# Optimization experiments

Measured on AMD Instinct MI355X. Metric: run time of the kernel, lower is better.

Reference implementation:

```python
import jax, jax.numpy as jnp
import numpy as np

B, T, N, C = 32, 12, 1024, 2   # batch, lookback window, n_series, in_channels
D, H, K, OUT = 16, 64, 2, 12   # embedding_dim, rnn_units, cheb_k, out_dim (horizon)


def setup_inputs() -> dict:
    key = jax.random.key(0)
    ks = jax.random.split(key, 12)
    p = lambda k, sh, s=0.1: jax.random.normal(k, sh, dtype=jnp.float32) * s
    return {
        "source": jax.random.normal(ks[0], (B, T, N, C), dtype=jnp.float32),
        "node_emb": p(ks[1], (N, D), 0.3),
        # layer 0: dim_in = C + H
        "gate_w0": p(ks[2], (D, K, C + H, 2 * H)),
        "gate_b0": p(ks[3], (D, 2 * H)),
        "upd_w0": p(ks[4], (D, K, C + H, H)),
        "upd_b0": p(ks[5], (D, H)),
        # layer 1: dim_in = H + H
        "gate_w1": p(ks[6], (D, K, 2 * H, 2 * H)),
        "gate_b1": p(ks[7], (D, 2 * H)),
        "upd_w1": p(ks[8], (D, K, 2 * H, H)),
        "upd_b1": p(ks[9], (D, H)),
        # end_conv: Conv2d(1, OUT*out_channels, kernel=(1,H)) == linear over hidden dim
        "conv_w": p(ks[10], (OUT, H)),
        "conv_b": p(ks[11], (OUT,)),
    }


def _supports(node_emb):
    # softmax(relu(E E^T)) row-normalized adaptive adjacency; Chebyshev stack (K, N, N)
    A = jax.nn.softmax(jax.nn.relu(node_emb @ node_emb.T), axis=1)
    s = [jnp.eye(N, dtype=A.dtype), A]
    for _ in range(2, K):
        s.append(2.0 * A @ s[-1] - s[-2])
    return jnp.stack(s, axis=0)


def _gcn(x, node_emb, w_pool, b_pool, supports):
    # x: (B, N, Cin); per-node adaptive weights from pools
    w = jnp.einsum('nd,dkio->nkio', node_emb, w_pool)     # (N, K, Cin, Cout)
    b = node_emb @ b_pool                                 # (N, Cout)
    xg = jnp.einsum('knm,bmc->bnkc', supports, x)         # (B, N, K, Cin)
    return jnp.einsum('bnki,nkio->bno', xg, w) + b


def _layer(x_seq, node_emb, supports, gw, gb, uw, ub):
    # x_seq: (B, T, N, Cin) -> (B, T, N, H) via GRU-style AGCRN cell, scanned over T
    def step(state, x_t):
        inp = jnp.concatenate([x_t, state], axis=-1)
        zr = jax.nn.sigmoid(_gcn(inp, node_emb, gw, gb, supports))
        z, r = jnp.split(zr, 2, axis=-1)
        cand = jnp.concatenate([x_t, z * state], axis=-1)
        hc = jnp.tanh(_gcn(cand, node_emb, uw, ub, supports))
        h = r * state + (1.0 - r) * hc
        return h, h

    init = jnp.zeros((x_seq.shape[0], N, H), dtype=x_seq.dtype)
    _, hs = jax.lax.scan(step, init, jnp.swapaxes(x_seq, 0, 1))
    return jnp.swapaxes(hs, 0, 1)


def reference(source, node_emb, gate_w0, gate_b0, upd_w0, upd_b0,
              gate_w1, gate_b1, upd_w1, upd_b1, conv_w, conv_b,
              teacher_forcing_ratio=0):
    sup = _supports(node_emb)  # adaptive supports depend only on static node_emb
    h1 = _layer(source, node_emb, sup, gate_w0, gate_b0, upd_w0, upd_b0)
    h2 = _layer(h1, node_emb, sup, gate_w1, gate_b1, upd_w1, upd_b1)
    last = h2[:, -1]  # (B, N, H)
    # end_conv over hidden dim -> (B, OUT, N); out_channels==1 so squeeze folds away
    out = jnp.einsum('bnh,oh->bon', last, conv_w) + conv_b[None, :, None]
    return out
```

## Files before the change

kernel.cpp:

```cpp
#include <hip/hip_runtime.h>
#include <hip/hip_fp16.h>


typedef _Float16 f16x8 __attribute__((ext_vector_type(8)));
typedef _Float16 f16x4 __attribute__((ext_vector_type(4)));
typedef float f32x4 __attribute__((ext_vector_type(4)));

__global__ __launch_bounds__(256) void compute_A_kernel(const float* __restrict__ E,
                                                        __half* __restrict__ Ah) {
  int n = blockIdx.x;
  int tid = threadIdx.x;
  __shared__ float red[256];
  float en[16];
#pragma unroll
  for (int d = 0; d < 16; ++d) en[d] = E[n * 16 + d];
  float v[4];
#pragma unroll
  for (int q = 0; q < 4; ++q) {
    int m = tid + q * 256;
    const float* Em = E + m * 16;
    float dot = 0.f;
#pragma unroll
    for (int d = 0; d < 16; ++d) dot += en[d] * Em[d];
    v[q] = fmaxf(dot, 0.f);
  }
  float mx = fmaxf(fmaxf(v[0], v[1]), fmaxf(v[2], v[3]));
  red[tid] = mx; __syncthreads();
  for (int s = 128; s > 0; s >>= 1) { if (tid < s) red[tid] = fmaxf(red[tid], red[tid + s]); __syncthreads(); }
  mx = red[0];
  __syncthreads();
  float e[4], sum = 0.f;
#pragma unroll
  for (int q = 0; q < 4; ++q) { e[q] = expf(v[q] - mx); sum += e[q]; }
  red[tid] = sum; __syncthreads();
  for (int s = 128; s > 0; s >>= 1) { if (tid < s) red[tid] += red[tid + s]; __syncthreads(); }
  float inv = 1.f / red[0];
#pragma unroll
  for (int q = 0; q < 4; ++q) Ah[(size_t)n * 1024 + tid + q * 256] = __float2half(e[q] * inv);
}

__global__ void build_e16_kernel(const float* __restrict__ E, __half* __restrict__ E16) {
  int t = blockIdx.x * 256 + threadIdx.x;
  if (t >= 1024 * 32) return;
  int d = t & 31;
  E16[t] = (d < 16) ? __float2half(E[(t >> 5) * 16 + d]) : __half(0);
}

__global__ void pool_t16_kernel(const float* __restrict__ gw0, const float* __restrict__ uw0,
                                const float* __restrict__ gw1, const float* __restrict__ uw1,
                                __half* __restrict__ poolT16) {
  int t = blockIdx.x * 256 + threadIdx.x;
  if (t >= 79872 * 32) return;
  int d = t & 31, j = t >> 5;
  if (d >= 16) { poolT16[t] = __half(0); return; }
  const float* pool; int F, Fp, O, loc;
  if (j < 20480)      { pool = gw0; F = 66;  Fp = 80;  O = 128; loc = j; }
  else if (j < 30720) { pool = uw0; F = 66;  Fp = 80;  O = 64;  loc = j - 20480; }
  else if (j < 63488) { pool = gw1; F = 128; Fp = 128; O = 128; loc = j - 30720; }
  else                { pool = uw1; F = 128; Fp = 128; O = 64;  loc = j - 63488; }
  int KIp = 2 * Fp;
  int o = loc / KIp, kip = loc - o * KIp;
  int kk = (kip >= Fp) ? 1 : 0;
  int jj = kip - kk * Fp;
  int i;
  if (F == Fp) i = jj;
  else i = (jj < 64) ? jj + 2 : (jj < 66 ? jj - 64 : -1);
  poolT16[t] = (i >= 0) ? __float2half(pool[(((size_t)d * 2 + kk) * F + i) * O + o]) : __half(0);
}

__global__ __launch_bounds__(256) void make_wt_mfma_kernel(
    const __half* __restrict__ E16g, const __half* __restrict__ poolT16g,
    __half* __restrict__ WtG0, __half* __restrict__ WtU0,
    __half* __restrict__ WtG1, __half* __restrict__ WtU1) {
  __shared__ __align__(16) _Float16 Es[64][40];
  __shared__ __align__(16) _Float16 wbuf[64][264];
  const _Float16* E16 = (const _Float16*)E16g;
  const _Float16* pT = (const _Float16*)poolT16g;
  int bx = blockIdx.x;
  __half* Wt; int OK, jbase;
  if (bx < 80)       { Wt = WtG0; OK = 128 * 160; jbase = bx * 256; }
  else if (bx < 120) { Wt = WtU0; OK = 64 * 160;  jbase = (bx - 80) * 256; }
  else if (bx < 248) { Wt = WtG1; OK = 128 * 256; jbase = (bx - 120) * 256; }
  else               { Wt = WtU1; OK = 64 * 256;  jbase = (bx - 248) * 256; }
  int jglob0 = bx * 256;
  int n0 = blockIdx.y * 64;
  {
    int r = threadIdx.x >> 2, ch = (threadIdx.x & 3) * 8;
    *(f16x8*)&Es[r][ch] = *(const f16x8*)(E16 + (size_t)(n0 + r) * 32 + ch);
  }
  __syncthreads();
  int wave = threadIdx.x >> 6, lane = threadIdx.x & 63;
  int fm = lane & 15, fg = lane >> 4;
  f16x8 af[4];
#pragma unroll
  for (int i = 0; i < 4; ++i) af[i] = *(const f16x8*)&Es[i * 16 + fm][fg * 8];
  f32x4 acc[4][4] = {};
#pragma unroll
  for (int j = 0; j < 4; ++j) {
    int jc = jglob0 + wave * 64 + j * 16 + fm;
    f16x8 bf = *(const f16x8*)(pT + (size_t)jc * 32 + fg * 8);
#pragma unroll
    for (int i = 0; i < 4; ++i)
      acc[i][j] = __builtin_amdgcn_mfma_f32_16x16x32_f16(af[i], bf, acc[i][j], 0, 0, 0);
  }
#pragma unroll
  for (int i = 0; i < 4; ++i)
#pragma unroll
    for (int j = 0; j < 4; ++j)
#pragma unroll
      for (int r = 0; r < 4; ++r)
        wbuf[i * 16 + fg * 4 + r][wave * 64 + j * 16 + fm] = (_Float16)acc[i][j][r];
  __syncthreads();
  for (int idx = threadIdx.x; idx < 64 * 32; idx += 256) {
    int nsub = idx >> 5, pos = (idx & 31) * 8;
    *(float4*)(Wt + (size_t)(n0 + nsub) * OK + jbase + pos) = *(float4*)&wbuf[nsub][pos];
  }
}

__global__ void make_b_all_kernel(const float* __restrict__ E,
                                  const float* __restrict__ gb0, const float* __restrict__ ub0,
                                  const float* __restrict__ gb1, const float* __restrict__ ub1,
                                  float* __restrict__ Bg0, float* __restrict__ Bu0,
                                  float* __restrict__ Bg1, float* __restrict__ Bu1) {
  int tid = blockIdx.x * 256 + threadIdx.x;
  if (tid >= 1024 * 384) return;
  int n = tid / 384, c = tid - n * 384;
  const float* pool; float* outp; int O, o;
  if (c < 128)      { pool = gb0; outp = Bg0; O = 128; o = c; }
  else if (c < 192) { pool = ub0; outp = Bu0; O = 64;  o = c - 128; }
  else if (c < 320) { pool = gb1; outp = Bg1; O = 128; o = c - 192; }
  else              { pool = ub1; outp = Bu1; O = 64;  o = c - 320; }
  const float* En = E + n * 16;
  float a = 0.f;
#pragma unroll
  for (int d = 0; d < 16; ++d) a += En[d] * pool[d * O + o];
  outp[n * O + o] = a;
}

__global__ void zero_kernel(float* __restrict__ p, int count) {
  int i = blockIdx.x * 256 + threadIdx.x;
  if (i < count) p[i] = 0.f;
}

__global__ void build_x16_kernel(const float* __restrict__ src, __half* __restrict__ x16) {
  int bid = blockIdx.x; int t = bid >> 5, b = bid & 31;
  const float* s = src + (size_t)(b * 12 + t) * 2048;
  __half* dst = x16 + t * 64 + b * 2;
  for (int n = threadIdx.x; n < 1024; n += 256) {
    float2 v = *(const float2*)(s + n * 2);
    *(__half2*)(dst + (size_t)n * 768) = __floats2half2_rn(v.x, v.y);
  }
}

__global__ __launch_bounds__(256) void gemm_nt_kernel(
    const __half* __restrict__ Ahg, const __half* __restrict__ X0g,
    const __half* __restrict__ X1g, __half* __restrict__ Yg,
    int Nc, int cstride, int split) {
  __shared__ __align__(16) _Float16 As[64][136];
  __shared__ __align__(16) _Float16 Bs[64][144];
  const _Float16* __restrict__ Ah = (const _Float16*)Ahg;
  _Float16* __restrict__ Y = (_Float16*)Yg;
  int tid = threadIdx.x;
  int row0 = blockIdx.y * 64;
  int col0 = blockIdx.x * 64;
  const _Float16* __restrict__ Xsrc =
      (col0 < split) ? (const _Float16*)X0g : (const _Float16*)X1g;
  int colg = (col0 < split) ? col0 : col0 - split;
  int wave = tid >> 6, lane = tid & 63;
  int wm = wave & 1, wn = wave >> 1;
  int fm = lane & 15, fg = lane >> 4;

  int sr = tid >> 2, sc = (tid & 3) * 32;
  const _Float16* pa = Ah + (size_t)(row0 + sr) * 1024 + sc;
  int kq = tid & 31, cg = tid >> 5;
  int kb = 4 * kq;
  const _Float16* pb = Xsrc + (size_t)kb * cstride + colg + cg * 8;
  int chunk = kq >> 1;
  int kin = (kq & 1) * 4;

  f16x8 ra[4], rb[4];
#pragma unroll
  for (int c = 0; c < 4; ++c) ra[c] = *(const f16x8*)(pa + c * 8);
#pragma unroll
  for (int r = 0; r < 4; ++r) rb[r] = *(const f16x8*)(pb + (size_t)r * cstride);

  f32x4 acc[2][2] = {};
  for (int k0 = 0; k0 < 1024; k0 += 128) {
#pragma unroll
    for (int c = 0; c < 4; ++c) *(f16x8*)&As[sr][sc + c * 8] = ra[c];
#pragma unroll
    for (int i = 0; i < 8; ++i) {
      int c = cg * 8 + i;
      f16x4 p;
      p[0] = rb[0][i]; p[1] = rb[1][i]; p[2] = rb[2][i]; p[3] = rb[3][i];
      *(f16x4*)&Bs[c][((chunk ^ (c & 7)) << 3) + kin] = p;
    }
    __syncthreads();
    if (k0 + 128 < 1024) {
#pragma unroll
      for (int c = 0; c < 4; ++c) ra[c] = *(const f16x8*)(pa + k0 + 128 + c * 8);
#pragma unroll
      for (int r = 0; r < 4; ++r)
        rb[r] = *(const f16x8*)(pb + (size_t)(k0 + 128 + r) * cstride);
    }
#pragma unroll
    for (int kc = 0; kc < 4; ++kc) {
      int ck = kc * 4 + fg;
      f16x8 af[2], bf[2];
#pragma unroll
      for (int i = 0; i < 2; ++i)
        af[i] = *(const f16x8*)&As[wm * 32 + i * 16 + fm][kc * 32 + fg * 8];
#pragma unroll
      for (int j = 0; j < 2; ++j) {
        int cl = wn * 32 + j * 16 + fm;
        bf[j] = *(const f16x8*)&Bs[cl][(ck ^ (cl & 7)) << 3];
      }
#pragma unroll
      for (int i = 0; i < 2; ++i)
#pragma unroll
        for (int j = 0; j < 2; ++j)
          acc[i][j] = __builtin_amdgcn_mfma_f32_16x16x32_f16(af[i], bf[j], acc[i][j], 0, 0, 0);
    }
    __syncthreads();
  }
#pragma unroll
  for (int i = 0; i < 2; ++i) {
#pragma unroll
    for (int j = 0; j < 2; ++j) {
      int col = col0 + wn * 32 + j * 16 + fm;
      int rbase = row0 + wm * 32 + i * 16 + fg * 4;
#pragma unroll
      for (int r = 0; r < 4; ++r)
        Y[(size_t)(rbase + r) * Nc + col] = (_Float16)acc[i][j][r];
    }
  }
}

__global__ __launch_bounds__(256) void gemm_nt128_kernel(
    const __half* __restrict__ Ahg, const __half* __restrict__ X0g,
    const __half* __restrict__ X1g, __half* __restrict__ Yg,
    int Nc, int cstride, int split) {
  __shared__ __align__(16) _Float16 As[64][136];
  __shared__ __align__(16) _Float16 Bs[128][144];
  const _Float16* __restrict__ Ah = (const _Float16*)Ahg;
  _Float16* __restrict__ Y = (_Float16*)Yg;
  int tid = threadIdx.x;
  int row0 = blockIdx.y * 64;
  int col0 = blockIdx.x * 128;
  const _Float16* __restrict__ Xsrc =
      (col0 < split) ? (const _Float16*)X0g : (const _Float16*)X1g;
  int colg = (col0 < split) ? col0 : col0 - split;
  int wave = tid >> 6, lane = tid & 63;
  int fm = lane & 15, fg = lane >> 4;

  int sr = tid >> 2, sc = (tid & 3) * 32;
  const _Float16* pa = Ah + (size_t)(row0 + sr) * 1024 + sc;
  int kq = tid & 31, cg = tid >> 5;
  int kb = 4 * kq;
  const _Float16* pb = Xsrc + (size_t)kb * cstride + colg + cg * 16;
  int chunk = kq >> 1;
  int kin = (kq & 1) * 4;

  f16x8 ra[4], rb[4][2];
#pragma unroll
  for (int c = 0; c < 4; ++c) ra[c] = *(const f16x8*)(pa + c * 8);
#pragma unroll
  for (int r = 0; r < 4; ++r)
#pragma unroll
    for (int h = 0; h < 2; ++h)
      rb[r][h] = *(const f16x8*)(pb + (size_t)r * cstride + h * 8);

  f32x4 acc[4][2] = {};
  for (int k0 = 0; k0 < 1024; k0 += 128) {
#pragma unroll
    for (int c = 0; c < 4; ++c) *(f16x8*)&As[sr][sc + c * 8] = ra[c];
#pragma unroll
    for (int h = 0; h < 2; ++h)
#pragma unroll
      for (int i = 0; i < 8; ++i) {
        int c = cg * 16 + h * 8 + i;
        f16x4 p;
        p[0] = rb[0][h][i]; p[1] = rb[1][h][i]; p[2] = rb[2][h][i]; p[3] = rb[3][h][i];
        *(f16x4*)&Bs[c][((chunk ^ (c & 7)) << 3) + kin] = p;
      }
    __syncthreads();
    if (k0 + 128 < 1024) {
#pragma unroll
      for (int c = 0; c < 4; ++c) ra[c] = *(const f16x8*)(pa + k0 + 128 + c * 8);
#pragma unroll
      for (int r = 0; r < 4; ++r)
#pragma unroll
        for (int h = 0; h < 2; ++h)
          rb[r][h] = *(const f16x8*)(pb + (size_t)(k0 + 128 + r) * cstride + h * 8);
    }
#pragma unroll
    for (int kc = 0; kc < 4; ++kc) {
      int ck = kc * 4 + fg;
      f16x8 af[4], bf[2];
#pragma unroll
      for (int i = 0; i < 4; ++i)
        af[i] = *(const f16x8*)&As[i * 16 + fm][kc * 32 + fg * 8];
#pragma unroll
      for (int j = 0; j < 2; ++j) {
        int cl = wave * 32 + j * 16 + fm;
        bf[j] = *(const f16x8*)&Bs[cl][(ck ^ (cl & 7)) << 3];
      }
#pragma unroll
      for (int i = 0; i < 4; ++i)
#pragma unroll
        for (int j = 0; j < 2; ++j)
          acc[i][j] = __builtin_amdgcn_mfma_f32_16x16x32_f16(af[i], bf[j], acc[i][j], 0, 0, 0);
    }
    __syncthreads();
  }
#pragma unroll
  for (int i = 0; i < 4; ++i) {
#pragma unroll
    for (int j = 0; j < 2; ++j) {
      int col = col0 + wave * 32 + j * 16 + fm;
      int rbase = row0 + i * 16 + fg * 4;
#pragma unroll
      for (int r = 0; r < 4; ++r)
        Y[(size_t)(rbase + r) * Nc + col] = (_Float16)acc[i][j][r];
    }
  }
}

__device__ __forceinline__ void gate0_body(
    _Float16* Xs, int n, int t,
    const __half* __restrict__ h16, const __half* __restrict__ YBD,
    const float* __restrict__ src, const __half* __restrict__ Axt, int tstep,
    const __half* __restrict__ Wtg, const float* __restrict__ Bg,
    const float* __restrict__ h32, __half* __restrict__ zh0, float* __restrict__ r0) {
  constexpr int KIP = 160, STRIDE = 168;
#pragma unroll
  for (int u = 0; u < 2; ++u) {
    int idx = t + u * 256;
    int b = idx >> 4, part = (idx >> 3) & 1, ch = idx & 7;
    const _Float16* s = part ? (const _Float16*)YBD + (size_t)n * 4096 + b * 64 + ch * 8
                             : (const _Float16*)h16 + (size_t)n * 2048 + b * 64 + ch * 8;
    *(f16x8*)&Xs[b * STRIDE + part * 80 + ch * 8] = *(const f16x8*)s;
  }
  if (t < 32) {
    int b = t;
    float2 xv = *(const float2*)(src + ((size_t)(b * 12 + tstep) * 1024 + n) * 2);
    Xs[b * STRIDE + 64] = (_Float16)xv.x;
    Xs[b * STRIDE + 65] = (_Float16)xv.y;
    const _Float16* ax = (const _Float16*)Axt + (size_t)n * 768 + tstep * 64 + b * 2;
    Xs[b * STRIDE + 144] = ax[0];
    Xs[b * STRIDE + 145] = ax[1];
  }
  for (int idx = t; idx < 896; idx += 256) {
    int b = idx / 28, jj = idx % 28;
    int col = (jj < 14) ? 66 + jj : 132 + jj;
    Xs[b * STRIDE + col] = (_Float16)0.f;
  }
  __syncthreads();
  int wave = t >> 6, lane = t & 63;
  int fm = lane & 15, fg = lane >> 4;
  f32x4 acc[2][2] = {};
  const _Float16* Wn = (const _Float16*)Wtg + ((size_t)n * 128 + wave * 32) * KIP;
#pragma unroll
  for (int kc = 0; kc < KIP / 32; ++kc) {
    f16x8 af[2], bf[2];
#pragma unroll
    for (int i = 0; i < 2; ++i)
      af[i] = *(const f16x8*)&Xs[(i * 16 + fm) * STRIDE + kc * 32 + fg * 8];
#pragma unroll
    for (int j = 0; j < 2; ++j)
      bf[j] = *(const f16x8*)(Wn + (size_t)(j * 16 + fm) * KIP + kc * 32 + fg * 8);
#pragma unroll
    for (int i = 0; i < 2; ++i)
#pragma unroll
      for (int j = 0; j < 2; ++j)
        acc[i][j] = __builtin_amdgcn_mfma_f32_16x16x32_f16(af[i], bf[j], acc[i][j], 0, 0, 0);
  }
  const float* Bn = Bg + n * 128;
#pragma unroll
  for (int j = 0; j < 2; ++j) {
    int o = wave * 32 + j * 16 + fm;
    float bias = Bn[o];
#pragma unroll
    for (int i = 0; i < 2; ++i)
#pragma unroll
      for (int r = 0; r < 4; ++r) {
        int b = i * 16 + fg * 4 + r;
        float s = 1.f / (1.f + __expf(-(acc[i][j][r] + bias)));
        size_t base = (size_t)n * 2048 + b * 64;
        if (o < 64) zh0[base + o] = __float2half(s * h32[base + o]);
        else        r0[base + o - 64] = s;
      }
  }
}

__device__ __forceinline__ void upd0_body(
    _Float16* Xs, int n, int t,
    const __half* __restrict__ zh0, const __half* __restrict__ YCE,
    const float* __restrict__ src, const __half* __restrict__ Axt, int tstep,
    const __half* __restrict__ Wtg, const float* __restrict__ Bu,
    const float* __restrict__ r0, float* __restrict__ h32, __half* __restrict__ h16) {
  constexpr int KIP = 160, STRIDE = 168;
#pragma unroll
  for (int u = 0; u < 2; ++u) {
    int idx = t + u * 256;
    int b = idx >> 4, part = (idx >> 3) & 1, ch = idx & 7;
    const _Float16* s = part ? (const _Float16*)YCE + (size_t)n * 4096 + 2048 + b * 64 + ch * 8
                             : (const _Float16*)zh0 + (size_t)n * 2048 + b * 64 + ch * 8;
    *(f16x8*)&Xs[b * STRIDE + part * 80 + ch * 8] = *(const f16x8*)s;
  }
  if (t < 32) {
    int b = t;
    float2 xv = *(const float2*)(src + ((size_t)(b * 12 + tstep) * 1024 + n) * 2);
    Xs[b * STRIDE + 64] = (_Float16)xv.x;
    Xs[b * STRIDE + 65] = (_Float16)xv.y;
    const _Float16* ax = (const _Float16*)Axt + (size_t)n * 768 + tstep * 64 + b * 2;
    Xs[b * STRIDE + 144] = ax[0];
    Xs[b * STRIDE + 145] = ax[1];
  }
  for (int idx = t; idx < 896; idx += 256) {
    int b = idx / 28, jj = idx % 28;
    int col = (jj < 14) ? 66 + jj : 132 + jj;
    Xs[b * STRIDE + col] = (_Float16)0.f;
  }
  __syncthreads();
  int wave = t >> 6, lane = t & 63;
  int fm = lane & 15, fg = lane >> 4;
  f32x4 acc[2] = {};
  const _Float16* Wn = (const _Float16*)Wtg + ((size_t)n * 64 + wave * 16) * KIP;
#pragma unroll
  for (int kc = 0; kc < KIP / 32; ++kc) {
    f16x8 bf = *(const f16x8*)(Wn + (size_t)fm * KIP + kc * 32 + fg * 8);
#pragma unroll
    for (int i = 0; i < 2; ++i) {
      f16x8 af = *(const f16x8*)&Xs[(i * 16 + fm) * STRIDE + kc * 32 + fg * 8];
      acc[i] = __builtin_amdgcn_mfma_f32_16x16x32_f16(af, bf, acc[i], 0, 0, 0);
    }
  }
  int o = wave * 16 + fm;
  float bias = Bu[n * 64 + o];
#pragma unroll
  for (int i = 0; i < 2; ++i)
#pragma unroll
    for (int r = 0; r < 4; ++r) {
      int b = i * 16 + fg * 4 + r;
      float x = acc[i][r] + bias;
      x = fminf(fmaxf(x, -15.f), 15.f);
      float e = __expf(2.f * x);
      float hc = (e - 1.f) / (e + 1.f);
      size_t base = (size_t)n * 2048 + b * 64;
      float rr = r0[base + o];
      float hnew = rr * h32[base + o] + (1.f - rr) * hc;
      h32[base + o] = hnew;
      h16[base + o] = __float2half(hnew);
    }
}

__global__ __launch_bounds__(256) void gate0_kernel(
    const __half* __restrict__ h16, const __half* __restrict__ YBD,
    const float* __restrict__ src, const __half* __restrict__ Axt, int tstep,
    const __half* __restrict__ Wtg, const float* __restrict__ Bg,
    const float* __restrict__ h32, __half* __restrict__ zh0, float* __restrict__ r0) {
  __shared__ __align__(16) _Float16 Xs[32 * 168];
  gate0_body(Xs, blockIdx.x, threadIdx.x, h16, YBD, src, Axt, tstep, Wtg, Bg, h32, zh0, r0);
}

__global__ __launch_bounds__(256) void upd0_kernel(
    const __half* __restrict__ zh0, const __half* __restrict__ YCE,
    const float* __restrict__ src, const __half* __restrict__ Axt, int tstep,
    const __half* __restrict__ Wtg, const float* __restrict__ Bu,
    const float* __restrict__ r0, float* __restrict__ h32, __half* __restrict__ h16) {
  __shared__ __align__(16) _Float16 Xs[32 * 168];
  upd0_body(Xs, blockIdx.x, threadIdx.x, zh0, YCE, src, Axt, tstep, Wtg, Bu, r0, h32, h16);
}

__global__ __launch_bounds__(256) void gate1_gate0_kernel(
    const __half* __restrict__ h1_16, const __half* __restrict__ h2_16,
    const __half* __restrict__ YBD,
    const __half* __restrict__ WtG1, const float* __restrict__ Bg1,
    const float* __restrict__ h2_32, __half* __restrict__ zh1, float* __restrict__ r1,
    const float* __restrict__ src, const __half* __restrict__ Axt, int tnext,
    const __half* __restrict__ WtG0, const float* __restrict__ Bg0,
    const float* __restrict__ h1_32, __half* __restrict__ zh0, float* __restrict__ r0,
    int do_gate0) {
  constexpr int KIP = 256, STRIDE = 264;
  __shared__ __align__(16) _Float16 Xs[32 * STRIDE];
  int n = blockIdx.x;
  int t = threadIdx.x;
#pragma unroll
  for (int u = 0; u < 4; ++u) {
    int idx = t + u * 256;
    int b = idx >> 5, q = idx & 31;
    const _Float16* s;
    if (q < 8)       s = (const _Float16*)h1_16 + (size_t)n * 2048 + b * 64 + q * 8;
    else if (q < 16) s = (const _Float16*)h2_16 + (size_t)n * 2048 + b * 64 + (q - 8) * 8;
    else if (q < 24) s = (const _Float16*)YBD + (size_t)n * 4096 + b * 64 + (q - 16) * 8;
    else             s = (const _Float16*)YBD + (size_t)n * 4096 + 2048 + b * 64 + (q - 24) * 8;
    *(f16x8*)&Xs[b * STRIDE + q * 8] = *(const f16x8*)s;
  }
  __syncthreads();
  int wave = t >> 6, lane = t & 63;
  int fm = lane & 15, fg = lane >> 4;
  {
    f32x4 acc[2][2] = {};
    const _Float16* Wn = (const _Float16*)WtG1 + ((size_t)n * 128 + wave * 32) * KIP;
#pragma unroll
    for (int kc = 0; kc < KIP / 32; ++kc) {
      f16x8 af[2], bf[2];
#pragma unroll
      for (int i = 0; i < 2; ++i)
        af[i] = *(const f16x8*)&Xs[(i * 16 + fm) * STRIDE + kc * 32 + fg * 8];
#pragma unroll
      for (int j = 0; j < 2; ++j)
        bf[j] = *(const f16x8*)(Wn + (size_t)(j * 16 + fm) * KIP + kc * 32 + fg * 8);
#pragma unroll
      for (int i = 0; i < 2; ++i)
#pragma unroll
        for (int j = 0; j < 2; ++j)
          acc[i][j] = __builtin_amdgcn_mfma_f32_16x16x32_f16(af[i], bf[j], acc[i][j], 0, 0, 0);
    }
    const float* Bn = Bg1 + n * 128;
#pragma unroll
    for (int j = 0; j < 2; ++j) {
      int o = wave * 32 + j * 16 + fm;
      float bias = Bn[o];
#pragma unroll
      for (int i = 0; i < 2; ++i)
#pragma unroll
        for (int r = 0; r < 4; ++r) {
          int b = i * 16 + fg * 4 + r;
          float s = 1.f / (1.f + __expf(-(acc[i][j][r] + bias)));
          size_t base = (size_t)n * 2048 + b * 64;
          if (o < 64) zh1[base + o] = __float2half(s * h2_32[base + o]);
          else        r1[base + o - 64] = s;
        }
    }
  }
  if (!do_gate0) return;
  __syncthreads();
  gate0_body(Xs, n, t, h1_16, YBD, src, Axt, tnext, WtG0, Bg0, h1_32, zh0, r0);
}

__global__ __launch_bounds__(256) void upd1_upd0_kernel(
    const __half* __restrict__ h1_16, const __half* __restrict__ zh1,
    const __half* __restrict__ YBD, const __half* __restrict__ YCE,
    const __half* __restrict__ WtU1, const float* __restrict__ Bu1,
    const float* __restrict__ r1, float* __restrict__ h2_32, __half* __restrict__ h2_16,
    const __half* __restrict__ zh0,
    const float* __restrict__ src, const __half* __restrict__ Axt, int tnext,
    const __half* __restrict__ WtU0, const float* __restrict__ Bu0,
    const float* __restrict__ r0, float* __restrict__ h1_32, __half* __restrict__ h1_16w,
    int do_upd0) {
  constexpr int KIP = 256, STRIDE = 264;
  __shared__ __align__(16) _Float16 Xs[32 * STRIDE];
  int n = blockIdx.x;
  int t = threadIdx.x;
#pragma unroll
  for (int u = 0; u < 4; ++u) {
    int idx = t + u * 256;
    int b = idx >> 5, q = idx & 31;
    const _Float16* s;
    if (q < 8)       s = (const _Float16*)h1_16 + (size_t)n * 2048 + b * 64 + q * 8;
    else if (q < 16) s = (const _Float16*)zh1 + (size_t)n * 2048 + b * 64 + (q - 8) * 8;
    else if (q < 24) s = (const _Float16*)YBD + (size_t)n * 4096 + b * 64 + (q - 16) * 8;
    else             s = (const _Float16*)YCE + (size_t)n * 4096 + b * 64 + (q - 24) * 8;
    *(f16x8*)&Xs[b * STRIDE + q * 8] = *(const f16x8*)s;
  }
  __syncthreads();
  int wave = t >> 6, lane = t & 63;
  int fm = lane & 15, fg = lane >> 4;
  {
    f32x4 acc[2] = {};
    const _Float16* Wn = (const _Float16*)WtU1 + ((size_t)n * 64 + wave * 16) * KIP;
#pragma unroll
    for (int kc = 0; kc < KIP / 32; ++kc) {
      f16x8 bf = *(const f16x8*)(Wn + (size_t)fm * KIP + kc * 32 + fg * 8);
#pragma unroll
      for (int i = 0; i < 2; ++i) {
        f16x8 af = *(const f16x8*)&Xs[(i * 16 + fm) * STRIDE + kc * 32 + fg * 8];
        acc[i] = __builtin_amdgcn_mfma_f32_16x16x32_f16(af, bf, acc[i], 0, 0, 0);
      }
    }
    int o = wave * 16 + fm;
    float bias = Bu1[n * 64 + o];
#pragma unroll
    for (int i = 0; i < 2; ++i)
#pragma unroll
      for (int r = 0; r < 4; ++r) {
        int b = i * 16 + fg * 4 + r;
        float x = acc[i][r] + bias;
        x = fminf(fmaxf(x, -15.f), 15.f);
        float e = __expf(2.f * x);
        float hc = (e - 1.f) / (e + 1.f);
        size_t base = (size_t)n * 2048 + b * 64;
        float rr = r1[base + o];
        float hnew = rr * h2_32[base + o] + (1.f - rr) * hc;
        h2_32[base + o] = hnew;
        h2_16[base + o] = __float2half(hnew);
      }
  }
  if (!do_upd0) return;
  __syncthreads();
  upd0_body(Xs, n, t, zh0, YCE, src, Axt, tnext, WtU0, Bu0, r0, h1_32, h1_16w);
}

__global__ void final_conv_kernel(const float* __restrict__ h2, const float* __restrict__ cw,
                                  const float* __restrict__ cb, float* __restrict__ out) {
  int tid = blockIdx.x * 256 + threadIdx.x;
  if (tid >= 32 * 1024) return;
  int n = tid & 1023, b = tid >> 10;
  const float* hp = h2 + ((size_t)n * 32 + b) * 64;
  float hv[64];
#pragma unroll
  for (int i = 0; i < 64; ++i) hv[i] = hp[i];
#pragma unroll
  for (int o = 0; o < 12; ++o) {
    float acc = cb[o];
#pragma unroll
    for (int i = 0; i < 64; ++i) acc += hv[i] * cw[o * 64 + i];
    out[((size_t)b * 12 + o) * 1024 + n] = acc;
  }
}

extern "C" void kernel_launch(void* const* d_in, const int* in_sizes, int n_in,
                              void* d_out, int out_size, void* d_ws, size_t ws_size,
                              hipStream_t stream) {
  const float* src = (const float*)d_in[0];
  const float* E   = (const float*)d_in[1];
  const float* gw0 = (const float*)d_in[2];
  const float* gb0 = (const float*)d_in[3];
  const float* uw0 = (const float*)d_in[4];
  const float* ub0 = (const float*)d_in[5];
  const float* gw1 = (const float*)d_in[6];
  const float* gb1 = (const float*)d_in[7];
  const float* uw1 = (const float*)d_in[8];
  const float* ub1 = (const float*)d_in[9];
  const float* cw  = (const float*)d_in[10];
  const float* cb  = (const float*)d_in[11];
  float* out = (float*)d_out;
  (void)in_sizes; (void)n_in; (void)out_size; (void)ws_size;

  char* base = (char*)d_ws;
  size_t off = 0;
  auto alloc = [&](size_t bytes) -> void* {
    void* p = base + off; off += (bytes + 511) & ~(size_t)511; return p;
  };
  __half* Ah   = (__half*)alloc((size_t)1024 * 1024 * 2);
  __half* WtG0 = (__half*)alloc((size_t)1024 * 128 * 160 * 2);
  __half* WtU0 = (__half*)alloc((size_t)1024 * 64 * 160 * 2);
  __half* WtG1 = (__half*)alloc((size_t)1024 * 128 * 256 * 2);
  __half* WtU1 = (__half*)alloc((size_t)1024 * 64 * 256 * 2);
  float*  Bg0  = (float*) alloc((size_t)1024 * 128 * 4);
  float*  Bu0  = (float*) alloc((size_t)1024 * 64 * 4);
  float*  Bg1  = (float*) alloc((size_t)1024 * 128 * 4);
  float*  Bu1  = (float*) alloc((size_t)1024 * 64 * 4);
  float*  h1_32 = (float*)alloc((size_t)1024 * 2048 * 4);
  float*  h2_32 = (float*)alloc((size_t)1024 * 2048 * 4);
  __half* h1_16 = (__half*)alloc((size_t)1024 * 2048 * 2);
  __half* h2_16 = (__half*)alloc((size_t)1024 * 2048 * 2);
  __half* YBD  = (__half*)alloc((size_t)1024 * 4096 * 2);
  __half* YCE  = (__half*)alloc((size_t)1024 * 4096 * 2);
  __half* zh0  = (__half*)alloc((size_t)1024 * 2048 * 2);
  __half* zh1  = (__half*)alloc((size_t)1024 * 2048 * 2);
  __half* Axt  = (__half*)alloc((size_t)1024 * 768 * 2);
  float*  r1   = (float*) alloc((size_t)1024 * 2048 * 4);
  float*  r0   = (float*) alloc((size_t)1024 * 2048 * 4);
  __half* poolT16 = (__half*)r0;
  __half* E16  = poolT16 + (size_t)79872 * 32;
  __half* x16  = E16 + (size_t)1024 * 32;

  compute_A_kernel<<<1024, 256, 0, stream>>>(E, Ah);
  build_e16_kernel<<<(1024 * 32 + 255) / 256, 256, 0, stream>>>(E, E16);
  pool_t16_kernel<<<(79872 * 32 + 255) / 256, 256, 0, stream>>>(gw0, uw0, gw1, uw1, poolT16);
  make_wt_mfma_kernel<<<dim3(312, 16), 256, 0, stream>>>(E16, poolT16, WtG0, WtU0, WtG1, WtU1);
  make_b_all_kernel<<<(1024 * 384 + 255) / 256, 256, 0, stream>>>(E, gb0, ub0, gb1, ub1,
                                                                  Bg0, Bu0, Bg1, Bu1);
  build_x16_kernel<<<384, 256, 0, stream>>>(src, x16);
  gemm_nt_kernel<<<dim3(12, 16), 256, 0, stream>>>(Ah, (__half*)x16, (__half*)x16, Axt,
                                                   768, 768, 768);
  zero_kernel<<<(8388608 + 255) / 256, 256, 0, stream>>>(h1_32, 8388608);

  gate0_kernel<<<1024, 256, 0, stream>>>(h1_16, YBD, src, Axt, 0, WtG0, Bg0, h1_32, zh0, r0);
  gemm_nt128_kernel<<<dim3(16, 16), 256, 0, stream>>>(Ah, zh0, zh0, YCE + 2048,
                                                      4096, 2048, 2048);
  upd0_kernel<<<1024, 256, 0, stream>>>(zh0, YCE, src, Axt, 0, WtU0, Bu0, r0, h1_32, h1_16);

  for (int t = 0; t < 12; ++t) {
    int more = (t < 11) ? 1 : 0;
    gemm_nt128_kernel<<<dim3(32, 16), 256, 0, stream>>>(Ah, h1_16, h2_16, YBD,
                                                        4096, 2048, 2048);
    gate1_gate0_kernel<<<1024, 256, 0, stream>>>(h1_16, h2_16, YBD, WtG1, Bg1, h2_32, zh1, r1,
                                                 src, Axt, t + 1, WtG0, Bg0, h1_32, zh0, r0,
                                                 more);
    gemm_nt128_kernel<<<dim3(32, 16), 256, 0, stream>>>(Ah, zh1, zh0, YCE,
                                                        4096, 2048, 2048);
    upd1_upd0_kernel<<<1024, 256, 0, stream>>>(h1_16, zh1, YBD, YCE, WtU1, Bu1, r1,
                                               h2_32, h2_16, zh0, src, Axt, t + 1,
                                               WtU0, Bu0, r0, h1_32, h1_16, more);
  }

  final_conv_kernel<<<(32 * 1024 + 255) / 256, 256, 0, stream>>>(h2_32, cw, cb, out);
}
```

Baseline: 1.398 ms.

## Merge prelude kernels, hoist gate/update loads, store r in fp16, raise MFMA priority

Combines the zeroing, x16 build, bias build and E16 build into one launch and rewrites pool_t16 so each thread writes vectorized 32-element rows. In the fused step kernels, the second stage's global loads are issued before the first GEMM so their latency overlaps it. The reset gate r is stored in half precision to halve its traffic, and the MFMA loops are wrapped in s_setprio. Intermediate buffers get separate allocations instead of aliasing r0. The fp16 r adds a small rounding error.

```diff
diff --git a/kernel.cpp b/kernel.cpp
--- a/kernel.cpp
+++ b/kernel.cpp
@@ -39,33 +39,88 @@
   for (int q = 0; q < 4; ++q) Ah[(size_t)n * 1024 + tid + q * 256] = __float2half(e[q] * inv);
 }
 
-__global__ void build_e16_kernel(const float* __restrict__ E, __half* __restrict__ E16) {
-  int t = blockIdx.x * 256 + threadIdx.x;
-  if (t >= 1024 * 32) return;
-  int d = t & 31;
-  E16[t] = (d < 16) ? __float2half(E[(t >> 5) * 16 + d]) : __half(0);
-}
-
-__global__ void pool_t16_kernel(const float* __restrict__ gw0, const float* __restrict__ uw0,
-                                const float* __restrict__ gw1, const float* __restrict__ uw1,
-                                __half* __restrict__ poolT16) {
-  int t = blockIdx.x * 256 + threadIdx.x;
-  if (t >= 79872 * 32) return;
-  int d = t & 31, j = t >> 5;
-  if (d >= 16) { poolT16[t] = __half(0); return; }
-  const float* pool; int F, Fp, O, loc;
-  if (j < 20480)      { pool = gw0; F = 66;  Fp = 80;  O = 128; loc = j; }
-  else if (j < 30720) { pool = uw0; F = 66;  Fp = 80;  O = 64;  loc = j - 20480; }
-  else if (j < 63488) { pool = gw1; F = 128; Fp = 128; O = 128; loc = j - 30720; }
-  else                { pool = uw1; F = 128; Fp = 128; O = 64;  loc = j - 63488; }
-  int KIp = 2 * Fp;
-  int o = loc / KIp, kip = loc - o * KIp;
-  int kk = (kip >= Fp) ? 1 : 0;
-  int jj = kip - kk * Fp;
+__global__ __launch_bounds__(256) void pool_t16_kernel(const float* __restrict__ gw0,
+                                                       const float* __restrict__ uw0,
+                                                       const float* __restrict__ gw1,
+                                                       const float* __restrict__ uw1,
+                                                       __half* __restrict__ poolT16) {
+  int rg = blockIdx.x;
+  const float* pool; int F, Fp, O; size_t jbase; int kk, jj;
+  if (rg < 160)      { pool = gw0; F = 66;  Fp = 80;  O = 128; jbase = 0;     kk = rg / 80;          jj = rg % 80; }
+  else if (rg < 320) { pool = uw0; F = 66;  Fp = 80;  O = 64;  jbase = 20480; kk = (rg - 160) / 80;  jj = (rg - 160) % 80; }
+  else if (rg < 576) { pool = gw1; F = 128; Fp = 128; O = 128; jbase = 30720; kk = (rg - 320) / 128; jj = (rg - 320) % 128; }
+  else               { pool = uw1; F = 128; Fp = 128; O = 64;  jbase = 63488; kk = (rg - 576) / 128; jj = (rg - 576) % 128; }
+  int o = threadIdx.x;
+  if (o >= O) return;
   int i;
   if (F == Fp) i = jj;
   else i = (jj < 64) ? jj + 2 : (jj < 66 ? jj - 64 : -1);
-  poolT16[t] = (i >= 0) ? __float2half(pool[(((size_t)d * 2 + kk) * F + i) * O + o]) : __half(0);
+  f16x8 a = {}, b = {}, zz = {};
+  if (i >= 0) {
+#pragma unroll
+    for (int d = 0; d < 8; ++d)
+      a[d] = (_Float16)pool[(((size_t)d * 2 + kk) * F + i) * O + o];
+#pragma unroll
+    for (int d = 8; d < 16; ++d)
+      b[d - 8] = (_Float16)pool[(((size_t)d * 2 + kk) * F + i) * O + o];
+  }
+  size_t j = jbase + (size_t)o * (2 * Fp) + (size_t)kk * Fp + jj;
+  _Float16* outp = (_Float16*)poolT16 + j * 32;
+  *(f16x8*)outp = a;
+  *(f16x8*)(outp + 8) = b;
+  *(f16x8*)(outp + 16) = zz;
+  *(f16x8*)(outp + 24) = zz;
+}
+
+__global__ __launch_bounds__(256) void prelude_misc_kernel(
+    const float* __restrict__ E, __half* __restrict__ E16,
+    const float* __restrict__ gb0, const float* __restrict__ ub0,
+    const float* __restrict__ gb1, const float* __restrict__ ub1,
+    float* __restrict__ Bg0, float* __restrict__ Bu0,
+    float* __restrict__ Bg1, float* __restrict__ Bu1,
+    const float* __restrict__ src, __half* __restrict__ x16,
+    float4* __restrict__ zero_p) {
+  int bid = blockIdx.x;
+  if (bid < 8192) {
+    int i = bid * 256 + threadIdx.x;
+    zero_p[i] = float4{0.f, 0.f, 0.f, 0.f};
+    return;
+  }
+  bid -= 8192;
+  if (bid < 384) {
+    int t0 = bid >> 5, b = bid & 31;
+    const float* s = src + (size_t)(b * 12 + t0) * 2048;
+    __half* dst = x16 + t0 * 64 + b * 2;
+    for (int nn = threadIdx.x; nn < 1024; nn += 256) {
+      float2 v = *(const float2*)(s + nn * 2);
+      *(__half2*)(dst + (size_t)nn * 768) = __floats2half2_rn(v.x, v.y);
+    }
+    return;
+  }
+  bid -= 384;
+  if (bid < 1536) {
+    int tid = bid * 256 + threadIdx.x;
+    if (tid >= 1024 * 384) return;
+    int n = tid / 384, c = tid - n * 384;
+    const float* pool; float* outp; int O, o;
+    if (c < 128)      { pool = gb0; outp = Bg0; O = 128; o = c; }
+    else if (c < 192) { pool = ub0; outp = Bu0; O = 64;  o = c - 128; }
+    else if (c < 320) { pool = gb1; outp = Bg1; O = 128; o = c - 192; }
+    else              { pool = ub1; outp = Bu1; O = 64;  o = c - 320; }
+    const float* En = E + n * 16;
+    float a = 0.f;
+#pragma unroll
+    for (int d = 0; d < 16; ++d) a += En[d] * pool[d * O + o];
+    outp[n * O + o] = a;
+    return;
+  }
+  bid -= 1536;
+  {
+    int t = bid * 256 + threadIdx.x;
+    if (t >= 1024 * 32) return;
+    int d = t & 31;
+    E16[t] = (d < 16) ? __float2half(E[(t >> 5) * 16 + d]) : __half(0);
+  }
 }
 
 __global__ __launch_bounds__(256) void make_wt_mfma_kernel(
@@ -117,41 +172,6 @@
   }
 }
 
-__global__ void make_b_all_kernel(const float* __restrict__ E,
-                                  const float* __restrict__ gb0, const float* __restrict__ ub0,
-                                  const float* __restrict__ gb1, const float* __restrict__ ub1,
-                                  float* __restrict__ Bg0, float* __restrict__ Bu0,
-                                  float* __restrict__ Bg1, float* __restrict__ Bu1) {
-  int tid = blockIdx.x * 256 + threadIdx.x;
-  if (tid >= 1024 * 384) return;
-  int n = tid / 384, c = tid - n * 384;
-  const float* pool; float* outp; int O, o;
-  if (c < 128)      { pool = gb0; outp = Bg0; O = 128; o = c; }
-  else if (c < 192) { pool = ub0; outp = Bu0; O = 64;  o = c - 128; }
-  else if (c < 320) { pool = gb1; outp = Bg1; O = 128; o = c - 192; }
-  else              { pool = ub1; outp = Bu1; O = 64;  o = c - 320; }
-  const float* En = E + n * 16;
-  float a = 0.f;
-#pragma unroll
-  for (int d = 0; d < 16; ++d) a += En[d] * pool[d * O + o];
-  outp[n * O + o] = a;
-}
-
-__global__ void zero_kernel(float* __restrict__ p, int count) {
-  int i = blockIdx.x * 256 + threadIdx.x;
-  if (i < count) p[i] = 0.f;
-}
-
-__global__ void build_x16_kernel(const float* __restrict__ src, __half* __restrict__ x16) {
-  int bid = blockIdx.x; int t = bid >> 5, b = bid & 31;
-  const float* s = src + (size_t)(b * 12 + t) * 2048;
-  __half* dst = x16 + t * 64 + b * 2;
-  for (int n = threadIdx.x; n < 1024; n += 256) {
-    float2 v = *(const float2*)(s + n * 2);
-    *(__half2*)(dst + (size_t)n * 768) = __floats2half2_rn(v.x, v.y);
-  }
-}
-
 __global__ __launch_bounds__(256) void gemm_nt_kernel(
     const __half* __restrict__ Ahg, const __half* __restrict__ X0g,
     const __half* __restrict__ X1g, __half* __restrict__ Yg,
@@ -326,29 +346,38 @@
   }
 }
 
+__device__ __forceinline__ f16x8 ld_g0(const __half* __restrict__ h16,
+                                       const __half* __restrict__ YBD, int n, int idx) {
+  int b = idx >> 4, part = (idx >> 3) & 1, ch = idx & 7;
+  const _Float16* s = part ? (const _Float16*)YBD + (size_t)n * 4096 + b * 64 + ch * 8
+                           : (const _Float16*)h16 + (size_t)n * 2048 + b * 64 + ch * 8;
+  return *(const f16x8*)s;
+}
+__device__ __forceinline__ f16x8 ld_u0(const __half* __restrict__ zh0,
+                                       const __half* __restrict__ YCE, int n, int idx) {
+  int b = idx >> 4, part = (idx >> 3) & 1, ch = idx & 7;
+  const _Float16* s = part ? (const _Float16*)YCE + (size_t)n * 4096 + 2048 + b * 64 + ch * 8
+                           : (const _Float16*)zh0 + (size_t)n * 2048 + b * 64 + ch * 8;
+  return *(const f16x8*)s;
+}
+
 __device__ __forceinline__ void gate0_body(
     _Float16* Xs, int n, int t,
-    const __half* __restrict__ h16, const __half* __restrict__ YBD,
-    const float* __restrict__ src, const __half* __restrict__ Axt, int tstep,
+    f16x8 pre0, f16x8 pre1, float2 xv, unsigned axu,
     const __half* __restrict__ Wtg, const float* __restrict__ Bg,
-    const float* __restrict__ h32, __half* __restrict__ zh0, float* __restrict__ r0) {
+    const float* __restrict__ h32, __half* __restrict__ zh0, __half* __restrict__ r0) {
   constexpr int KIP = 160, STRIDE = 168;
-#pragma unroll
-  for (int u = 0; u < 2; ++u) {
-    int idx = t + u * 256;
-    int b = idx >> 4, part = (idx >> 3) & 1, ch = idx & 7;
-    const _Float16* s = part ? (const _Float16*)YBD + (size_t)n * 4096 + b * 64 + ch * 8
-                             : (const _Float16*)h16 + (size_t)n * 2048 + b * 64 + ch * 8;
-    *(f16x8*)&Xs[b * STRIDE + part * 80 + ch * 8] = *(const f16x8*)s;
+  {
+    int b0 = t >> 4, p0 = (t >> 3) & 1, c0 = t & 7;
+    *(f16x8*)&Xs[b0 * STRIDE + p0 * 80 + c0 * 8] = pre0;
+    int idx = t + 256;
+    int b1 = idx >> 4, p1 = (idx >> 3) & 1, c1 = idx & 7;
+    *(f16x8*)&Xs[b1 * STRIDE + p1 * 80 + c1 * 8] = pre1;
   }
   if (t < 32) {
-    int b = t;
-    float2 xv = *(const float2*)(src + ((size_t)(b * 12 + tstep) * 1024 + n) * 2);
-    Xs[b * STRIDE + 64] = (_Float16)xv.x;
-    Xs[b * STRIDE + 65] = (_Float16)xv.y;
-    const _Float16* ax = (const _Float16*)Axt + (size_t)n * 768 + tstep * 64 + b * 2;
-    Xs[b * STRIDE + 144] = ax[0];
-    Xs[b * STRIDE + 145] = ax[1];
+    Xs[t * STRIDE + 64] = (_Float16)xv.x;
+    Xs[t * STRIDE + 65] = (_Float16)xv.y;
+    *(unsigned*)&Xs[t * STRIDE + 144] = axu;
   }
   for (int idx = t; idx < 896; idx += 256) {
     int b = idx / 28, jj = idx % 28;
@@ -360,6 +389,7 @@
   int fm = lane & 15, fg = lane >> 4;
   f32x4 acc[2][2] = {};
   const _Float16* Wn = (const _Float16*)Wtg + ((size_t)n * 128 + wave * 32) * KIP;
+  __builtin_amdgcn_s_setprio(1);
 #pragma unroll
   for (int kc = 0; kc < KIP / 32; ++kc) {
     f16x8 af[2], bf[2];
@@ -375,6 +405,7 @@
       for (int j = 0; j < 2; ++j)
         acc[i][j] = __builtin_amdgcn_mfma_f32_16x16x32_f16(af[i], bf[j], acc[i][j], 0, 0, 0);
   }
+  __builtin_amdgcn_s_setprio(0);
   const float* Bn = Bg + n * 128;
 #pragma unroll
   for (int j = 0; j < 2; ++j) {
@@ -388,34 +419,28 @@
         float s = 1.f / (1.f + __expf(-(acc[i][j][r] + bias)));
         size_t base = (size_t)n * 2048 + b * 64;
         if (o < 64) zh0[base + o] = __float2half(s * h32[base + o]);
-        else        r0[base + o - 64] = s;
+        else        r0[base + o - 64] = __float2half(s);
       }
   }
 }
 
 __device__ __forceinline__ void upd0_body(
     _Float16* Xs, int n, int t,
-    const __half* __restrict__ zh0, const __half* __restrict__ YCE,
-    const float* __restrict__ src, const __half* __restrict__ Axt, int tstep,
+    f16x8 pre0, f16x8 pre1, float2 xv, unsigned axu,
     const __half* __restrict__ Wtg, const float* __restrict__ Bu,
-    const float* __restrict__ r0, float* __restrict__ h32, __half* __restrict__ h16) {
+    const __half* __restrict__ r0, float* __restrict__ h32, __half* __restrict__ h16) {
   constexpr int KIP = 160, STRIDE = 168;
-#pragma unroll
-  for (int u = 0; u < 2; ++u) {
-    int idx = t + u * 256;
-    int b = idx >> 4, part = (idx >> 3) & 1, ch = idx & 7;
-    const _Float16* s = part ? (const _Float16*)YCE + (size_t)n * 4096 + 2048 + b * 64 + ch * 8
-                             : (const _Float16*)zh0 + (size_t)n * 2048 + b * 64 + ch * 8;
-    *(f16x8*)&Xs[b * STRIDE + part * 80 + ch * 8] = *(const f16x8*)s;
+  {
+    int b0 = t >> 4, p0 = (t >> 3) & 1, c0 = t & 7;
+    *(f16x8*)&Xs[b0 * STRIDE + p0 * 80 + c0 * 8] = pre0;
+    int idx = t + 256;
+    int b1 = idx >> 4, p1 = (idx >> 3) & 1, c1 = idx & 7;
+    *(f16x8*)&Xs[b1 * STRIDE + p1 * 80 + c1 * 8] = pre1;
   }
   if (t < 32) {
-    int b = t;
-    float2 xv = *(const float2*)(src + ((size_t)(b * 12 + tstep) * 1024 + n) * 2);
-    Xs[b * STRIDE + 64] = (_Float16)xv.x;
-    Xs[b * STRIDE + 65] = (_Float16)xv.y;
-    const _Float16* ax = (const _Float16*)Axt + (size_t)n * 768 + tstep * 64 + b * 2;
-    Xs[b * STRIDE + 144] = ax[0];
-    Xs[b * STRIDE + 145] = ax[1];
+    Xs[t * STRIDE + 64] = (_Float16)xv.x;
+    Xs[t * STRIDE + 65] = (_Float16)xv.y;
+    *(unsigned*)&Xs[t * STRIDE + 144] = axu;
   }
   for (int idx = t; idx < 896; idx += 256) {
     int b = idx / 28, jj = idx % 28;
@@ -427,6 +452,7 @@
   int fm = lane & 15, fg = lane >> 4;
   f32x4 acc[2] = {};
   const _Float16* Wn = (const _Float16*)Wtg + ((size_t)n * 64 + wave * 16) * KIP;
+  __builtin_amdgcn_s_setprio(1);
 #pragma unroll
   for (int kc = 0; kc < KIP / 32; ++kc) {
     f16x8 bf = *(const f16x8*)(Wn + (size_t)fm * KIP + kc * 32 + fg * 8);
@@ -436,6 +462,7 @@
       acc[i] = __builtin_amdgcn_mfma_f32_16x16x32_f16(af, bf, acc[i], 0, 0, 0);
     }
   }
+  __builtin_amdgcn_s_setprio(0);
   int o = wave * 16 + fm;
   float bias = Bu[n * 64 + o];
 #pragma unroll
@@ -448,7 +475,7 @@
       float e = __expf(2.f * x);
       float hc = (e - 1.f) / (e + 1.f);
       size_t base = (size_t)n * 2048 + b * 64;
-      float rr = r0[base + o];
+      float rr = __half2float(r0[base + o]);
       float hnew = rr * h32[base + o] + (1.f - rr) * hc;
       h32[base + o] = hnew;
       h16[base + o] = __float2half(hnew);
@@ -459,33 +486,50 @@
     const __half* __restrict__ h16, const __half* __restrict__ YBD,
     const float* __restrict__ src, const __half* __restrict__ Axt, int tstep,
     const __half* __restrict__ Wtg, const float* __restrict__ Bg,
-    const float* __restrict__ h32, __half* __restrict__ zh0, float* __restrict__ r0) {
+    const float* __restrict__ h32, __half* __restrict__ zh0, __half* __restrict__ r0) {
   __shared__ __align__(16) _Float16 Xs[32 * 168];
-  gate0_body(Xs, blockIdx.x, threadIdx.x, h16, YBD, src, Axt, tstep, Wtg, Bg, h32, zh0, r0);
+  int n = blockIdx.x, t = threadIdx.x;
+  f16x8 p0 = ld_g0(h16, YBD, n, t);
+  f16x8 p1 = ld_g0(h16, YBD, n, t + 256);
+  float2 xv = {}; unsigned ax = 0;
+  if (t < 32) {
+    xv = *(const float2*)(src + ((size_t)(t * 12 + tstep) * 1024 + n) * 2);
+    ax = *(const unsigned*)((const _Float16*)Axt + (size_t)n * 768 + tstep * 64 + t * 2);
+  }
+  gate0_body(Xs, n, t, p0, p1, xv, ax, Wtg, Bg, h32, zh0, r0);
 }
 
 __global__ __launch_bounds__(256) void upd0_kernel(
     const __half* __restrict__ zh0, const __half* __restrict__ YCE,
     const float* __restrict__ src, const __half* __restrict__ Axt, int tstep,
     const __half* __restrict__ Wtg, const float* __restrict__ Bu,
-    const float* __restrict__ r0, float* __restrict__ h32, __half* __restrict__ h16) {
+    const __half* __restrict__ r0, float* __restrict__ h32, __half* __restrict__ h16) {
   __shared__ __align__(16) _Float16 Xs[32 * 168];
-  upd0_body(Xs, blockIdx.x, threadIdx.x, zh0, YCE, src, Axt, tstep, Wtg, Bu, r0, h32, h16);
+  int n = blockIdx.x, t = threadIdx.x;
+  f16x8 p0 = ld_u0(zh0, YCE, n, t);
+  f16x8 p1 = ld_u0(zh0, YCE, n, t + 256);
+  float2 xv = {}; unsigned ax = 0;
+  if (t < 32) {
+    xv = *(const float2*)(src + ((size_t)(t * 12 + tstep) * 1024 + n) * 2);
+    ax = *(const unsigned*)((const _Float16*)Axt + (size_t)n * 768 + tstep * 64 + t * 2);
+  }
+  upd0_body(Xs, n, t, p0, p1, xv, ax, Wtg, Bu, r0, h32, h16);
 }
 
 __global__ __launch_bounds__(256) void gate1_gate0_kernel(
     const __half* __restrict__ h1_16, const __half* __restrict__ h2_16,
     const __half* __restrict__ YBD,
     const __half* __restrict__ WtG1, const float* __restrict__ Bg1,
-    const float* __restrict__ h2_32, __half* __restrict__ zh1, float* __restrict__ r1,
+    const float* __restrict__ h2_32, __half* __restrict__ zh1, __half* __restrict__ r1,
     const float* __restrict__ src, const __half* __restrict__ Axt, int tnext,
     const __half* __restrict__ WtG0, const float* __restrict__ Bg0,
-    const float* __restrict__ h1_32, __half* __restrict__ zh0, float* __restrict__ r0,
+    const float* __restrict__ h1_32, __half* __restrict__ zh0, __half* __restrict__ r0,
     int do_gate0) {
   constexpr int KIP = 256, STRIDE = 264;
   __shared__ __align__(16) _Float16 Xs[32 * STRIDE];
   int n = blockIdx.x;
   int t = threadIdx.x;
+  f16x8 s1[4];
 #pragma unroll
   for (int u = 0; u < 4; ++u) {
     int idx = t + u * 256;
@@ -495,7 +539,22 @@
     else if (q < 16) s = (const _Float16*)h2_16 + (size_t)n * 2048 + b * 64 + (q - 8) * 8;
     else if (q < 24) s = (const _Float16*)YBD + (size_t)n * 4096 + b * 64 + (q - 16) * 8;
     else             s = (const _Float16*)YBD + (size_t)n * 4096 + 2048 + b * 64 + (q - 24) * 8;
-    *(f16x8*)&Xs[b * STRIDE + q * 8] = *(const f16x8*)s;
+    s1[u] = *(const f16x8*)s;
+  }
+  f16x8 g0p0 = {}, g0p1 = {}; float2 g0xv = {}; unsigned g0ax = 0;
+  if (do_gate0) {
+    g0p0 = ld_g0(h1_16, YBD, n, t);
+    g0p1 = ld_g0(h1_16, YBD, n, t + 256);
+    if (t < 32) {
+      g0xv = *(const float2*)(src + ((size_t)(t * 12 + tnext) * 1024 + n) * 2);
+      g0ax = *(const unsigned*)((const _Float16*)Axt + (size_t)n * 768 + tnext * 64 + t * 2);
+    }
+  }
+#pragma unroll
+  for (int u = 0; u < 4; ++u) {
+    int idx = t + u * 256;
+    int b = idx >> 5, q = idx & 31;
+    *(f16x8*)&Xs[b * STRIDE + q * 8] = s1[u];
   }
   __syncthreads();
   int wave = t >> 6, lane = t & 63;
@@ -503,6 +562,7 @@
   {
     f32x4 acc[2][2] = {};
     const _Float16* Wn = (const _Float16*)WtG1 + ((size_t)n * 128 + wave * 32) * KIP;
+    __builtin_amdgcn_s_setprio(1);
 #pragma unroll
     for (int kc = 0; kc < KIP / 32; ++kc) {
       f16x8 af[2], bf[2];
@@ -518,6 +578,7 @@
         for (int j = 0; j < 2; ++j)
           acc[i][j] = __builtin_amdgcn_mfma_f32_16x16x32_f16(af[i], bf[j], acc[i][j], 0, 0, 0);
     }
+    __builtin_amdgcn_s_setprio(0);
     const float* Bn = Bg1 + n * 128;
 #pragma unroll
     for (int j = 0; j < 2; ++j) {
@@ -531,29 +592,30 @@
           float s = 1.f / (1.f + __expf(-(acc[i][j][r] + bias)));
           size_t base = (size_t)n * 2048 + b * 64;
           if (o < 64) zh1[base + o] = __float2half(s * h2_32[base + o]);
-          else        r1[base + o - 64] = s;
+          else        r1[base + o - 64] = __float2half(s);
         }
     }
   }
   if (!do_gate0) return;
   __syncthreads();
-  gate0_body(Xs, n, t, h1_16, YBD, src, Axt, tnext, WtG0, Bg0, h1_32, zh0, r0);
+  gate0_body(Xs, n, t, g0p0, g0p1, g0xv, g0ax, WtG0, Bg0, h1_32, zh0, r0);
 }
 
 __global__ __launch_bounds__(256) void upd1_upd0_kernel(
     const __half* __restrict__ h1_16, const __half* __restrict__ zh1,
     const __half* __restrict__ YBD, const __half* __restrict__ YCE,
     const __half* __restrict__ WtU1, const float* __restrict__ Bu1,
-    const float* __restrict__ r1, float* __restrict__ h2_32, __half* __restrict__ h2_16,
+    const __half* __restrict__ r1, float* __restrict__ h2_32, __half* __restrict__ h2_16,
     const __half* __restrict__ zh0,
     const float* __restrict__ src, const __half* __restrict__ Axt, int tnext,
     const __half* __restrict__ WtU0, const float* __restrict__ Bu0,
-    const float* __restrict__ r0, float* __restrict__ h1_32, __half* __restrict__ h1_16w,
+    const __half* __restrict__ r0, float* __restrict__ h1_32, __half* __restrict__ h1_16w,
     int do_upd0) {
   constexpr int KIP = 256, STRIDE = 264;
   __shared__ __align__(16) _Float16 Xs[32 * STRIDE];
   int n = blockIdx.x;
   int t = threadIdx.x;
+  f16x8 s1[4];
 #pragma unroll
   for (int u = 0; u < 4; ++u) {
     int idx = t + u * 256;
@@ -563,7 +625,22 @@
     else if (q < 16) s = (const _Float16*)zh1 + (size_t)n * 2048 + b * 64 + (q - 8) * 8;
     else if (q < 24) s = (const _Float16*)YBD + (size_t)n * 4096 + b * 64 + (q - 16) * 8;
     else             s = (const _Float16*)YCE + (size_t)n * 4096 + b * 64 + (q - 24) * 8;
-    *(f16x8*)&Xs[b * STRIDE + q * 8] = *(const f16x8*)s;
+    s1[u] = *(const f16x8*)s;
+  }
+  f16x8 u0p0 = {}, u0p1 = {}; float2 u0xv = {}; unsigned u0ax = 0;
+  if (do_upd0) {
+    u0p0 = ld_u0(zh0, YCE, n, t);
+    u0p1 = ld_u0(zh0, YCE, n, t + 256);
+    if (t < 32) {
+      u0xv = *(const float2*)(src + ((size_t)(t * 12 + tnext) * 1024 + n) * 2);
+      u0ax = *(const unsigned*)((const _Float16*)Axt + (size_t)n * 768 + tnext * 64 + t * 2);
+    }
+  }
+#pragma unroll
+  for (int u = 0; u < 4; ++u) {
+    int idx = t + u * 256;
+    int b = idx >> 5, q = idx & 31;
+    *(f16x8*)&Xs[b * STRIDE + q * 8] = s1[u];
   }
   __syncthreads();
   int wave = t >> 6, lane = t & 63;
@@ -571,6 +648,7 @@
   {
     f32x4 acc[2] = {};
     const _Float16* Wn = (const _Float16*)WtU1 + ((size_t)n * 64 + wave * 16) * KIP;
+    __builtin_amdgcn_s_setprio(1);
 #pragma unroll
     for (int kc = 0; kc < KIP / 32; ++kc) {
       f16x8 bf = *(const f16x8*)(Wn + (size_t)fm * KIP + kc * 32 + fg * 8);
@@ -580,6 +658,7 @@
         acc[i] = __builtin_amdgcn_mfma_f32_16x16x32_f16(af, bf, acc[i], 0, 0, 0);
       }
     }
+    __builtin_amdgcn_s_setprio(0);
     int o = wave * 16 + fm;
     float bias = Bu1[n * 64 + o];
 #pragma unroll
@@ -592,7 +671,7 @@
         float e = __expf(2.f * x);
         float hc = (e - 1.f) / (e + 1.f);
         size_t base = (size_t)n * 2048 + b * 64;
-        float rr = r1[base + o];
+        float rr = __half2float(r1[base + o]);
         float hnew = rr * h2_32[base + o] + (1.f - rr) * hc;
         h2_32[base + o] = hnew;
         h2_16[base + o] = __float2half(hnew);
@@ -600,7 +679,7 @@
   }
   if (!do_upd0) return;
   __syncthreads();
-  upd0_body(Xs, n, t, zh0, YCE, src, Axt, tnext, WtU0, Bu0, r0, h1_32, h1_16w);
+  upd0_body(Xs, n, t, u0p0, u0p1, u0xv, u0ax, WtU0, Bu0, r0, h1_32, h1_16w);
 }
 
 __global__ void final_conv_kernel(const float* __restrict__ h2, const float* __restrict__ cw,
@@ -662,22 +741,20 @@
   __half* zh0  = (__half*)alloc((size_t)1024 * 2048 * 2);
   __half* zh1  = (__half*)alloc((size_t)1024 * 2048 * 2);
   __half* Axt  = (__half*)alloc((size_t)1024 * 768 * 2);
-  float*  r1   = (float*) alloc((size_t)1024 * 2048 * 4);
-  float*  r0   = (float*) alloc((size_t)1024 * 2048 * 4);
-  __half* poolT16 = (__half*)r0;
-  __half* E16  = poolT16 + (size_t)79872 * 32;
-  __half* x16  = E16 + (size_t)1024 * 32;
+  __half* r1   = (__half*)alloc((size_t)1024 * 2048 * 2);
+  __half* r0   = (__half*)alloc((size_t)1024 * 2048 * 2);
+  __half* poolT16 = (__half*)alloc((size_t)79872 * 32 * 2);
+  __half* E16  = (__half*)alloc((size_t)1024 * 32 * 2);
+  __half* x16  = (__half*)alloc((size_t)1024 * 768 * 2);
 
   compute_A_kernel<<<1024, 256, 0, stream>>>(E, Ah);
-  build_e16_kernel<<<(1024 * 32 + 255) / 256, 256, 0, stream>>>(E, E16);
-  pool_t16_kernel<<<(79872 * 32 + 255) / 256, 256, 0, stream>>>(gw0, uw0, gw1, uw1, poolT16);
+  prelude_misc_kernel<<<10240, 256, 0, stream>>>(E, E16, gb0, ub0, gb1, ub1,
+                                                 Bg0, Bu0, Bg1, Bu1,
+                                                 src, x16, (float4*)h1_32);
+  pool_t16_kernel<<<832, 256, 0, stream>>>(gw0, uw0, gw1, uw1, poolT16);
   make_wt_mfma_kernel<<<dim3(312, 16), 256, 0, stream>>>(E16, poolT16, WtG0, WtU0, WtG1, WtU1);
-  make_b_all_kernel<<<(1024 * 384 + 255) / 256, 256, 0, stream>>>(E, gb0, ub0, gb1, ub1,
-                                                                  Bg0, Bu0, Bg1, Bu1);
-  build_x16_kernel<<<384, 256, 0, stream>>>(src, x16);
   gemm_nt_kernel<<<dim3(12, 16), 256, 0, stream>>>(Ah, (__half*)x16, (__half*)x16, Axt,
                                                    768, 768, 768);
-  zero_kernel<<<(8388608 + 255) / 256, 256, 0, stream>>>(h1_32, 8388608);
 
   gate0_kernel<<<1024, 256, 0, stream>>>(h1_16, YBD, src, Axt, 0, WtG0, Bg0, h1_32, zh0, r0);
   gemm_nt128_kernel<<<dim3(16, 16), 256, 0, stream>>>(Ah, zh0, zh0, YCE + 2048,
```

Result: no change. 1.377 ms (-1.5%).
